# Kernel optimization log

Measured on AMD Instinct MI355X. Metric: run time of the kernel, lower is better.

Reference implementation:

```python
import jax, jax.numpy as jnp
import numpy as np
import math

C = 512          # channels
K = 3            # conv kernel size
DILATIONS = (1, 3, 5)
RATIO = 2        # up/down sample ratio
FK = 12          # FIR anti-alias kernel size


def kaiser_sinc_filter1d(cutoff, half_width, kernel_size):
    # BigVGAN alias-free kaiser-windowed sinc lowpass filter
    half_size = kernel_size // 2
    delta_f = 4.0 * half_width
    A = 2.285 * (half_size - 1) * math.pi * delta_f + 7.95
    if A > 50.0:
        beta = 0.1102 * (A - 8.7)
    elif A >= 21.0:
        beta = 0.5842 * (A - 21.0) ** 0.4 + 0.07886 * (A - 21.0)
    else:
        beta = 0.0
    window = np.kaiser(kernel_size, beta)
    if kernel_size % 2 == 0:
        time = np.arange(-half_size, half_size) + 0.5
    else:
        time = np.arange(kernel_size) - half_size
    filt = 2.0 * cutoff * window * np.sinc(2.0 * cutoff * time)
    filt = filt / filt.sum()
    return jnp.asarray(filt, dtype=jnp.float32)

# Up/Down both use cutoff=0.5/ratio, half_width=0.6/ratio, kernel=12
AA_FILTER = kaiser_sinc_filter1d(0.5 / RATIO, 0.6 / RATIO, FK)

UP_PAD = FK // RATIO - 1                               # 5 (replicate pad before transpose conv)
UP_PAD_LEFT = UP_PAD * RATIO + (FK - RATIO) // 2       # 15
UP_PAD_RIGHT = UP_PAD * RATIO + (FK - RATIO + 1) // 2  # 15
DN_PAD_LEFT = FK // 2 - 1                              # 5 (even kernel)
DN_PAD_RIGHT = FK // 2                                 # 6


def _depthwise_conv(x, filt, stride=1, lhs_dilation=1, padding=(0, 0)):
    c = x.shape[1]
    w = jnp.broadcast_to(filt.reshape(1, 1, -1), (c, 1, filt.shape[0]))
    return jax.lax.conv_general_dilated(
        x, w, window_strides=(stride,), padding=[padding],
        lhs_dilation=(lhs_dilation,), dimension_numbers=('NCH', 'OIH', 'NCH'),
        feature_group_count=c)


def upsample2x(x):
    # replicate pad, depthwise transposed conv (lhs-dilated conv w/ flipped kernel), crop, scale
    x = jnp.pad(x, ((0, 0), (0, 0), (UP_PAD, UP_PAD)), mode='edge')
    y = RATIO * _depthwise_conv(x, AA_FILTER[::-1], lhs_dilation=RATIO,
                                padding=(FK - 1, FK - 1))
    return y[..., UP_PAD_LEFT:-UP_PAD_RIGHT]


def downsample2x(x):
    x = jnp.pad(x, ((0, 0), (0, 0), (DN_PAD_LEFT, DN_PAD_RIGHT)), mode='edge')
    return _depthwise_conv(x, AA_FILTER, stride=RATIO)


def snake_log(x, alpha, beta):
    # use_log_scale=True: alpha/beta are exponentiated; x + 1/(b+1e-5) * sin(a*x)^2
    a = jnp.exp(alpha)[None, :, None]
    b = jnp.exp(beta)[None, :, None]
    return x + (1.0 / (b + 1e-5)) * jnp.square(jnp.sin(x * a))


def aliasing_activation(x, alpha, beta):
    return downsample2x(snake_log(upsample2x(x), alpha, beta))


def weight_norm_conv1d(x, v, g, bias, dilation):
    # torch weight_norm dim=0: W[o] = g[o] * v[o] / ||v[o]||
    norm = jnp.sqrt(jnp.sum(v * v, axis=(1, 2), keepdims=True))
    w = g[:, None, None] * v / norm
    pad = (K * dilation - dilation) // 2
    y = jax.lax.conv_general_dilated(
        x, w, window_strides=(1,), padding=[(pad, pad)],
        rhs_dilation=(dilation,), dimension_numbers=('NCH', 'OIH', 'NCH'))
    return y + bias[None, :, None]


def setup_inputs() -> dict:
    key = jax.random.key(0)
    ks = jax.random.split(key, 12)
    B, T = 16, 4096
    return {
        'x': jax.random.normal(ks[0], (B, C, T), dtype=jnp.float32),
        'float_masks': jnp.ones((B, 1, T), dtype=jnp.float32),
        'in_snake_alpha': 0.1 * jax.random.normal(ks[1], (3, C), dtype=jnp.float32),
        'in_snake_beta': 0.1 * jax.random.normal(ks[2], (3, C), dtype=jnp.float32),
        'out_snake_alpha': 0.1 * jax.random.normal(ks[3], (3, C), dtype=jnp.float32),
        'out_snake_beta': 0.1 * jax.random.normal(ks[4], (3, C), dtype=jnp.float32),
        'in_conv_v': 0.05 * jax.random.normal(ks[5], (3, C, C, K), dtype=jnp.float32),
        'in_conv_g': 1.0 + 0.01 * jax.random.normal(ks[6], (3, C), dtype=jnp.float32),
        'in_conv_b': 0.01 * jax.random.normal(ks[7], (3, C), dtype=jnp.float32),
        'out_conv_v': 0.05 * jax.random.normal(ks[8], (3, C, C, K), dtype=jnp.float32),
        'out_conv_g': 1.0 + 0.01 * jax.random.normal(ks[9], (3, C), dtype=jnp.float32),
        'out_conv_b': 0.01 * jax.random.normal(ks[10], (3, C), dtype=jnp.float32),
    }


def reference(x, float_masks, in_snake_alpha, in_snake_beta, out_snake_alpha,
              out_snake_beta, in_conv_v, in_conv_g, in_conv_b, out_conv_v,
              out_conv_g, out_conv_b):
    for i, dilation in enumerate(DILATIONS):
        residuals = x
        x = aliasing_activation(x, in_snake_alpha[i], in_snake_beta[i]) * float_masks
        x = weight_norm_conv1d(x, in_conv_v[i], in_conv_g[i], in_conv_b[i], dilation)
        x = aliasing_activation(x, out_snake_alpha[i], out_snake_beta[i]) * float_masks
        x = weight_norm_conv1d(x, out_conv_v[i], out_conv_g[i], out_conv_b[i], 1)
        x = x + residuals
    return x * float_masks
```

## Files before the change

### kernel.cpp

```cpp
#include <hip/hip_runtime.h>
#include <cmath>

#define BN_ 16
#define CN_ 512
#define TN_ 4096
#define TPAD_ 4112
#define PADR_ 8

typedef float f32x4 __attribute__((ext_vector_type(4)));
typedef __bf16 bf16x8 __attribute__((ext_vector_type(8)));
typedef unsigned short u16x8 __attribute__((ext_vector_type(8)));

struct AAFilt { float g0[6]; float g1[6]; float fE[6]; float fO[6]; };

__device__ __forceinline__ unsigned short f2bf(float f) {
  unsigned u = __builtin_bit_cast(unsigned, f);
  u = (u + 0x7fffu + ((u >> 16) & 1u)) >> 16;
  return (unsigned short)u;
}
__device__ __forceinline__ float bf2f(unsigned short h) {
  return __builtin_bit_cast(float, (unsigned)h << 16);
}

__device__ __forceinline__ void gld16(const void* g, void* l) {
  __builtin_amdgcn_global_load_lds((const __attribute__((address_space(1))) void*)g,
                                   (__attribute__((address_space(3))) void*)l,
                                   16, 0, 0);
}

__global__ __launch_bounds__(256) void prep_w(
    const float* __restrict__ vin, const float* __restrict__ gin,
    const float* __restrict__ vout, const float* __restrict__ gout,
    unsigned short* __restrict__ wpack)
{
  const int o = blockIdx.x;
  const int l = blockIdx.y;
  const int i = l >> 1, oc = l & 1;
  const float* v = (oc ? vout : vin) + (size_t)i * CN_ * CN_ * 3 + (size_t)o * CN_ * 3;
  const float g = (oc ? gout : gin)[i * CN_ + o];
  const int tid = threadIdx.x;

  float a = 0.f;
  for (int j = tid; j < 1536; j += 256) { float x = v[j]; a += x * x; }
  #pragma unroll
  for (int off = 32; off > 0; off >>= 1) a += __shfl_down(a, off);
  __shared__ float red[4];
  if ((tid & 63) == 0) red[tid >> 6] = a;
  __syncthreads();
  const float tot = red[0] + red[1] + red[2] + red[3];
  const float scale = g / sqrtf(tot);
  unsigned short* wl = wpack + (size_t)l * 3 * CN_ * CN_;
  for (int j = tid; j < 1536; j += 256) {
    int c = j / 3, k = j - 3 * c;
    wl[((size_t)k * CN_ + o) * CN_ + c] = f2bf(v[j] * scale);
  }
}

__global__ __launch_bounds__(256) void transpose_in(
    const float* __restrict__ src, unsigned short* __restrict__ dst)
{
  __shared__ float tile[32][33];
  const int b = blockIdx.z, c0 = blockIdx.y * 32, t0 = blockIdx.x * 32;
  const int tx = threadIdx.x & 31, ty = threadIdx.x >> 5;
  const float* s = src + ((size_t)b * CN_ + c0) * TN_ + t0;
  #pragma unroll
  for (int j = 0; j < 32; j += 8) tile[ty + j][tx] = s[(size_t)(ty + j) * TN_ + tx];
  __syncthreads();
  unsigned short* d = dst + ((size_t)b * TN_ + t0) * CN_ + c0;
  #pragma unroll
  for (int j = 0; j < 32; j += 8) d[(size_t)(ty + j) * CN_ + tx] = f2bf(tile[tx][ty + j]);
}

__global__ __launch_bounds__(512) void act_kernel(
    const unsigned short* __restrict__ src, unsigned short* __restrict__ dst,
    const float* __restrict__ alpha, const float* __restrict__ beta,
    const float* __restrict__ mask, AAFilt F)
{
  const int c = threadIdx.x;
  const int b = blockIdx.y;
  const int seg = blockIdx.x;
  const int t0 = seg << 7;
  const float av = expf(alpha[c]);
  const float ib = 1.0f / (expf(beta[c]) + 1e-5f);
  const unsigned short* row = src + (size_t)b * TN_ * CN_ + c;
  unsigned short* drow = dst + (size_t)b * TPAD_ * CN_ + c;
  const float* mrow = mask + (size_t)b * TN_;

  if (seg == 0)  { for (int p = 0; p < PADR_; ++p) drow[(size_t)p * CN_] = 0; }
  if (seg == 31) { for (int p = 0; p < PADR_; ++p) drow[(size_t)(TPAD_ - PADR_ + p) * CN_] = 0; }

  auto ldx = [&](int t) -> float {
    t = t < 0 ? 0 : (t > TN_ - 1 ? TN_ - 1 : t);
    return bf2f(row[(size_t)t * CN_]);
  };

  float xw[6];
  #pragma unroll
  for (int j = 0; j < 6; ++j) xw[j] = ldx(t0 - 5 + j);
  float sE[6], sO[6];
  #pragma unroll
  for (int j = 0; j < 6; ++j) { sE[j] = 0.f; sO[j] = 0.f; }
  float s_last = 0.f;

  auto step = [&](int tau, bool emit) {
    float uO = 0.f, uE = 0.f;
    #pragma unroll
    for (int j = 0; j < 6; ++j) { uO += F.g1[j] * xw[j]; uE += F.g0[j] * xw[j]; }
    float so = __sinf(uO * av); float sOn = uO + ib * so * so;
    float se = __sinf(uE * av); float sEn = uE + ib * se * se;
    if (tau + 2 == TN_ - 1) s_last = sOn;
    if (tau + 2 >= TN_) sOn = s_last;
    if (tau + 3 >= TN_) sEn = s_last;
    #pragma unroll
    for (int j = 0; j < 5; ++j) { sE[j] = sE[j + 1]; sO[j] = sO[j + 1]; }
    sE[5] = sEn; sO[5] = sOn;
    if (emit) {
      float d = 0.f;
      #pragma unroll
      for (int j = 0; j < 6; ++j) d += F.fE[j] * sE[j] + F.fO[j] * sO[j];
      d *= mrow[tau];
      drow[(size_t)(PADR_ + tau) * CN_] = f2bf(d);
    }
    #pragma unroll
    for (int j = 0; j < 5; ++j) xw[j] = xw[j + 1];
    xw[5] = ldx(tau + 6);
  };

  for (int w = 0; w < 5; ++w) step(t0 - 5 + w, false);
  if (t0 == 0) {
    float s0 = sE[3];
    sE[1] = s0; sE[2] = s0;
    sO[1] = s0; sO[2] = s0; sO[3] = s0;
  }
  for (int t = t0; t < t0 + 128; ++t) step(t, true);
}

#define ASZ (272 * 32)
#define BSZ (3 * 256 * 32)

#define VMCNT(n) asm volatile("s_waitcnt vmcnt(" #n ")" ::: "memory")
#define BAR __builtin_amdgcn_s_barrier()
#define PRIO1 __builtin_amdgcn_s_setprio(1)
#define PRIO0 __builtin_amdgcn_s_setprio(0)

#define READ_A(k, mlo) do { \
    const int rb_ = rbase[k] + (mlo) * 16; \
    const int q_ = q4 ^ ((rb_ >> 1) & 3); \
    const unsigned short* ap_ = A + ((size_t)rb_ * 4 + q_) * 8; \
    af[0] = __builtin_bit_cast(bf16x8, *(const u16x8*)(ap_)); \
    af[1] = __builtin_bit_cast(bf16x8, *(const u16x8*)(ap_ + 512)); \
    af[2] = __builtin_bit_cast(bf16x8, *(const u16x8*)(ap_ + 1024)); \
    af[3] = __builtin_bit_cast(bf16x8, *(const u16x8*)(ap_ + 1536)); \
  } while (0)

#define READ_B(k) do { \
    const int ob_ = wn * 64 + l15; \
    const int q_ = q4 ^ ((ob_ >> 1) & 3); \
    const unsigned short* bp_ = Bc + (((size_t)(k) * 256 + ob_) * 4 + q_) * 8; \
    bfr[0] = __builtin_bit_cast(bf16x8, *(const u16x8*)(bp_)); \
    bfr[1] = __builtin_bit_cast(bf16x8, *(const u16x8*)(bp_ + 512)); \
    bfr[2] = __builtin_bit_cast(bf16x8, *(const u16x8*)(bp_ + 1024)); \
    bfr[3] = __builtin_bit_cast(bf16x8, *(const u16x8*)(bp_ + 1536)); \
  } while (0)

#define MFMA16(mlo) do { \
    _Pragma("unroll") \
    for (int mi_ = 0; mi_ < 4; ++mi_) { \
      _Pragma("unroll") \
      for (int ni_ = 0; ni_ < 4; ++ni_) \
        acc[(mlo) + mi_][ni_] = __builtin_amdgcn_mfma_f32_16x16x32_bf16( \
            af[mi_], bfr[ni_], acc[(mlo) + mi_][ni_], 0, 0, 0); \
    } \
  } while (0)

template <int MODE, int DIL>
__global__ __launch_bounds__(512, 2) void conv_kernel(
    const unsigned short* __restrict__ act,
    const unsigned short* __restrict__ wp,
    const float* __restrict__ bias,
    const unsigned short* __restrict__ res,
    const float* __restrict__ mask,
    void* __restrict__ outp)
{
  __shared__ __align__(16) unsigned short lA[2 * ASZ];
  __shared__ __align__(16) unsigned short lB[2 * BSZ];

  const int tid = threadIdx.x;
  const int bid = blockIdx.x;
  const int xcd = bid & 7, j = bid >> 3;
  const int ob = j & 1, tile = j >> 1;
  const int tt = tile * 8 + xcd;
  const int b = tt >> 4;
  const int t0 = (tt & 15) << 8;
  const int o0 = ob << 8;

  const int lane = tid & 63;
  const int wave = tid >> 6;
  const int wm = wave >> 2, wn = wave & 3;
  const int l15 = lane & 15, q4 = lane >> 4;

  const f32x4 zero = {0.f, 0.f, 0.f, 0.f};
  f32x4 acc[8][4];
  #pragma unroll
  for (int a = 0; a < 8; ++a)
    #pragma unroll
    for (int n = 0; n < 4; ++n) acc[a][n] = zero;

  const unsigned short* aBase = act + ((size_t)b * TPAD_ + t0) * CN_;

  int rbase[3];
  #pragma unroll
  for (int k = 0; k < 3; ++k) rbase[k] = wm * 128 + l15 + PADR_ + (k - 1) * DIL;

  auto stageA = [&](unsigned short* Ad, int c0) {
    { int p = tid;       int r = p >> 2, pq = p & 3, gq = pq ^ ((r >> 1) & 3);
      gld16(aBase + (size_t)r * CN_ + c0 + gq * 8, Ad + (size_t)p * 8); }
    { int p = tid + 512; int r = p >> 2, pq = p & 3, gq = pq ^ ((r >> 1) & 3);
      gld16(aBase + (size_t)r * CN_ + c0 + gq * 8, Ad + (size_t)p * 8); }
    if (tid < 64) {
      int p = tid + 1024;
      int r = p >> 2, pq = p & 3, gq = pq ^ ((r >> 1) & 3);
      gld16(aBase + (size_t)r * CN_ + c0 + gq * 8, Ad + (size_t)p * 8); }
  };
  auto stageB = [&](unsigned short* Bd, int c0, int k) {
    { int p = tid;       int ol = p >> 2, pq = p & 3, gq = pq ^ ((ol >> 1) & 3);
      gld16(wp + ((size_t)(k * CN_) + o0 + ol) * CN_ + c0 + gq * 8,
            Bd + ((size_t)k * 1024 + p) * 8); }
    { int p = tid + 512; int ol = p >> 2, pq = p & 3, gq = pq ^ ((ol >> 1) & 3);
      gld16(wp + ((size_t)(k * CN_) + o0 + ol) * CN_ + c0 + gq * 8,
            Bd + ((size_t)k * 1024 + p) * 8); }
  };

  stageA(lA, 0); stageB(lB, 0, 0); stageB(lB, 0, 1); stageB(lB, 0, 2);
  VMCNT(4);
  BAR;

  for (int cb = 0; cb < 15; ++cb) {
    const unsigned short* A  = lA + (size_t)(cb & 1) * ASZ;
    const unsigned short* Bc = lB + (size_t)(cb & 1) * BSZ;
    unsigned short* An = lA + (size_t)((cb & 1) ^ 1) * ASZ;
    unsigned short* Bn = lB + (size_t)((cb & 1) ^ 1) * BSZ;
    const int c0n = (cb + 1) * 32;
    bf16x8 af[4], bfr[4];
    READ_A(0, 0); READ_B(0); stageA(An, c0n);
    BAR; PRIO1; MFMA16(0); PRIO0; BAR;
    READ_A(0, 4); stageB(Bn, c0n, 0);
    BAR; PRIO1; MFMA16(4); PRIO0; VMCNT(6); BAR;
    READ_A(1, 0); READ_B(1); stageB(Bn, c0n, 1);
    BAR; PRIO1; MFMA16(0); PRIO0; BAR;
    READ_A(1, 4); stageB(Bn, c0n, 2);
    BAR; PRIO1; MFMA16(4); PRIO0; VMCNT(6); BAR;
    READ_A(2, 0); READ_B(2);
    BAR; PRIO1; MFMA16(0); PRIO0; BAR;
    READ_A(2, 4);
    BAR; PRIO1; MFMA16(4); PRIO0; VMCNT(4); BAR;
  }
  {
    const unsigned short* A  = lA + ASZ;
    const unsigned short* Bc = lB + BSZ;
    bf16x8 af[4], bfr[4];
    READ_A(0, 0); READ_B(0);
    BAR; PRIO1; MFMA16(0); PRIO0; BAR;
    READ_A(0, 4);
    BAR; PRIO1; MFMA16(4); PRIO0; VMCNT(2); BAR;
    READ_A(1, 0); READ_B(1);
    BAR; PRIO1; MFMA16(0); PRIO0; BAR;
    READ_A(1, 4);
    BAR; PRIO1; MFMA16(4); PRIO0; VMCNT(0); BAR;
    READ_A(2, 0); READ_B(2);
    BAR; PRIO1; MFMA16(0); PRIO0; BAR;
    READ_A(2, 4);
    BAR; PRIO1; MFMA16(4); PRIO0;
  }

  const int obase = o0 + wn * 64 + l15;
  const int tbase = t0 + wm * 128 + q4 * 4;

  if (MODE == 0) {
    unsigned short* O = (unsigned short*)outp + (size_t)b * TN_ * CN_;
    #pragma unroll
    for (int ni = 0; ni < 4; ++ni) {
      float bv = bias[obase + ni * 16];
      #pragma unroll
      for (int mi = 0; mi < 8; ++mi) {
        #pragma unroll
        for (int r = 0; r < 4; ++r) {
          int t = tbase + mi * 16 + r;
          O[(size_t)t * CN_ + obase + ni * 16] = f2bf(acc[mi][ni][r] + bv);
        }
      }
    }
  } else if (MODE == 1) {
    unsigned short* O = (unsigned short*)outp + (size_t)b * TN_ * CN_;
    const unsigned short* R = res + (size_t)b * TN_ * CN_;
    #pragma unroll
    for (int ni = 0; ni < 4; ++ni) {
      float bv = bias[obase + ni * 16];
      #pragma unroll
      for (int mi = 0; mi < 8; ++mi) {
        #pragma unroll
        for (int r = 0; r < 4; ++r) {
          int t = tbase + mi * 16 + r;
          size_t ix = (size_t)t * CN_ + obase + ni * 16;
          O[ix] = f2bf(acc[mi][ni][r] + bv + bf2f(R[ix]));
        }
      }
    }
  } else {
    float* O = (float*)outp + (size_t)b * CN_ * TN_;
    const unsigned short* R = res + (size_t)b * TN_ * CN_;
    const float* M = mask + (size_t)b * TN_;
    float bv[4];
    #pragma unroll
    for (int ni = 0; ni < 4; ++ni) bv[ni] = bias[obase + ni * 16];
    #pragma unroll
    for (int mi = 0; mi < 8; ++mi) {
      int t = tbase + mi * 16;
      f32x4 mv = *reinterpret_cast<const f32x4*>(M + t);
      #pragma unroll
      for (int ni = 0; ni < 4; ++ni) {
        f32x4 v;
        #pragma unroll
        for (int r = 0; r < 4; ++r)
          v[r] = (acc[mi][ni][r] + bv[ni] + bf2f(R[(size_t)(t + r) * CN_ + obase + ni * 16])) * mv[r];
        *reinterpret_cast<f32x4*>(O + (size_t)(obase + ni * 16) * TN_ + t) = v;
      }
    }
  }
}

static double bi0(double x) {
  double s = 1.0, t = 1.0, q = x * x * 0.25;
  for (int k = 1; k < 50; ++k) { t *= q / ((double)k * (double)k); s += t; if (t < 1e-18 * s) break; }
  return s;
}
static void make_filt(AAFilt* F) {
  const double PI = 3.14159265358979323846;
  double A = 2.285 * 5.0 * PI * 1.2 + 7.95;
  double beta;
  if (A > 50.0) beta = 0.1102 * (A - 8.7);
  else if (A >= 21.0) beta = 0.5842 * pow(A - 21.0, 0.4) + 0.07886 * (A - 21.0);
  else beta = 0.0;
  double i0b = bi0(beta);
  double f[12], sum = 0.0;
  for (int n = 0; n < 12; ++n) {
    double xx = 2.0 * n / 11.0 - 1.0;
    double w = bi0(beta * sqrt(fmax(0.0, 1.0 - xx * xx))) / i0b;
    double tt = (double)(n - 6) + 0.5;
    double arg = 0.5 * tt;
    double snc = sin(PI * arg) / (PI * arg);
    f[n] = 0.5 * w * snc;
    sum += f[n];
  }
  for (int n = 0; n < 12; ++n) f[n] /= sum;
  for (int j = 0; j < 6; ++j) {
    F->g0[j] = (float)(2.0 * f[11 - 2 * j]);
    F->g1[j] = (float)(2.0 * f[10 - 2 * j]);
    F->fE[j] = (float)f[2 * j + 1];
    F->fO[j] = (float)f[2 * j];
  }
}

extern "C" void kernel_launch(void* const* d_in, const int* in_sizes, int n_in,
                              void* d_out, int out_size, void* d_ws, size_t ws_size,
                              hipStream_t stream)
{
  (void)in_sizes; (void)n_in; (void)out_size; (void)ws_size;
  const float* x    = (const float*)d_in[0];
  const float* mask = (const float*)d_in[1];
  const float* inA  = (const float*)d_in[2];
  const float* inB  = (const float*)d_in[3];
  const float* outA = (const float*)d_in[4];
  const float* outB = (const float*)d_in[5];
  const float* vin  = (const float*)d_in[6];
  const float* gin  = (const float*)d_in[7];
  const float* bin  = (const float*)d_in[8];
  const float* vout = (const float*)d_in[9];
  const float* gout = (const float*)d_in[10];
  const float* bout = (const float*)d_in[11];

  char* ws = (char*)d_ws;
  unsigned short* xta  = (unsigned short*)ws;
  unsigned short* xtb  = (unsigned short*)(ws + 67108864);
  unsigned short* actb = (unsigned short*)(ws + 134217728);
  unsigned short* y1   = (unsigned short*)(ws + 134217728 + 67371008);
  unsigned short* wpk  = (unsigned short*)(ws + 134217728 + 67371008 + 67108864);

  AAFilt F; make_filt(&F);

  prep_w<<<dim3(512, 6), dim3(256), 0, stream>>>(vin, gin, vout, gout, wpk);
  transpose_in<<<dim3(128, 16, 16), dim3(256), 0, stream>>>(x, xta);

  act_kernel<<<dim3(32, 16), dim3(512), 0, stream>>>(
      xta, actb, inA + 0 * CN_, inB + 0 * CN_, mask, F);
  conv_kernel<0, 1><<<dim3(512), dim3(512), 0, stream>>>(
      actb, wpk + (size_t)0 * 3 * CN_ * CN_, bin + 0 * CN_, nullptr, mask, (void*)y1);
  act_kernel<<<dim3(32, 16), dim3(512), 0, stream>>>(
      y1, actb, outA + 0 * CN_, outB + 0 * CN_, mask, F);
  conv_kernel<1, 1><<<dim3(512), dim3(512), 0, stream>>>(
      actb, wpk + (size_t)1 * 3 * CN_ * CN_, bout + 0 * CN_, xta, mask, (void*)xtb);

  act_kernel<<<dim3(32, 16), dim3(512), 0, stream>>>(
      xtb, actb, inA + 1 * CN_, inB + 1 * CN_, mask, F);
  conv_kernel<0, 3><<<dim3(512), dim3(512), 0, stream>>>(
      actb, wpk + (size_t)2 * 3 * CN_ * CN_, bin + 1 * CN_, nullptr, mask, (void*)y1);
  act_kernel<<<dim3(32, 16), dim3(512), 0, stream>>>(
      y1, actb, outA + 1 * CN_, outB + 1 * CN_, mask, F);
  conv_kernel<1, 1><<<dim3(512), dim3(512), 0, stream>>>(
      actb, wpk + (size_t)3 * 3 * CN_ * CN_, bout + 1 * CN_, xtb, mask, (void*)xta);

  act_kernel<<<dim3(32, 16), dim3(512), 0, stream>>>(
      xta, actb, inA + 2 * CN_, inB + 2 * CN_, mask, F);
  conv_kernel<0, 5><<<dim3(512), dim3(512), 0, stream>>>(
      actb, wpk + (size_t)4 * 3 * CN_ * CN_, bin + 2 * CN_, nullptr, mask, (void*)y1);
  act_kernel<<<dim3(32, 16), dim3(512), 0, stream>>>(
      y1, actb, outA + 2 * CN_, outB + 2 * CN_, mask, F);
  conv_kernel<2, 1><<<dim3(512), dim3(512), 0, stream>>>(
      actb, wpk + (size_t)5 * 3 * CN_ * CN_, bout + 2 * CN_, xta, mask, d_out);
}
```

Before: 1.150 ms.

## Restructure conv GEMM main loop into 64-channel k-tiles with per-tap A staging

```diff
diff --git a/kernel.cpp b/kernel.cpp
--- a/kernel.cpp
+++ b/kernel.cpp
@@ -1,5 +1,6 @@
 #include <hip/hip_runtime.h>
 #include <cmath>
+#include <cstddef>
 
 #define BN_ 16
 #define CN_ 512
@@ -135,41 +136,50 @@
   for (int t = t0; t < t0 + 128; ++t) step(t, true);
 }
 
-#define ASZ (272 * 32)
-#define BSZ (3 * 256 * 32)
+#define HSZ 8192
+#define TSZ 16384
 
 #define VMCNT(n) asm volatile("s_waitcnt vmcnt(" #n ")" ::: "memory")
 #define BAR __builtin_amdgcn_s_barrier()
 #define PRIO1 __builtin_amdgcn_s_setprio(1)
 #define PRIO0 __builtin_amdgcn_s_setprio(0)
 
-#define READ_A(k, mlo) do { \
-    const int rb_ = rbase[k] + (mlo) * 16; \
-    const int q_ = q4 ^ ((rb_ >> 1) & 3); \
-    const unsigned short* ap_ = A + ((size_t)rb_ * 4 + q_) * 8; \
-    af[0] = __builtin_bit_cast(bf16x8, *(const u16x8*)(ap_)); \
-    af[1] = __builtin_bit_cast(bf16x8, *(const u16x8*)(ap_ + 512)); \
-    af[2] = __builtin_bit_cast(bf16x8, *(const u16x8*)(ap_ + 1024)); \
-    af[3] = __builtin_bit_cast(bf16x8, *(const u16x8*)(ap_ + 1536)); \
+#define READ_A(base, mh) do { \
+    _Pragma("unroll") \
+    for (int mi_ = 0; mi_ < 4; ++mi_) { \
+      const int row_ = wm * 128 + (mh) * 64 + mi_ * 16 + l15; \
+      _Pragma("unroll") \
+      for (int kk_ = 0; kk_ < 2; ++kk_) { \
+        const int q_ = (q4 + kk_ * 4) ^ (row_ & 7); \
+        af[mi_][kk_] = __builtin_bit_cast(bf16x8, \
+            *(const u16x8*)((base) + (size_t)row_ * 64 + q_ * 8)); \
+      } \
+    } \
   } while (0)
 
-#define READ_B(k) do { \
-    const int ob_ = wn * 64 + l15; \
-    const int q_ = q4 ^ ((ob_ >> 1) & 3); \
-    const unsigned short* bp_ = Bc + (((size_t)(k) * 256 + ob_) * 4 + q_) * 8; \
-    bfr[0] = __builtin_bit_cast(bf16x8, *(const u16x8*)(bp_)); \
-    bfr[1] = __builtin_bit_cast(bf16x8, *(const u16x8*)(bp_ + 512)); \
-    bfr[2] = __builtin_bit_cast(bf16x8, *(const u16x8*)(bp_ + 1024)); \
-    bfr[3] = __builtin_bit_cast(bf16x8, *(const u16x8*)(bp_ + 1536)); \
+#define READ_B(base, nh) do { \
+    _Pragma("unroll") \
+    for (int ni_ = 0; ni_ < 2; ++ni_) { \
+      const int orow_ = wn * 64 + ((nh) * 2 + ni_) * 16 + l15; \
+      _Pragma("unroll") \
+      for (int kk_ = 0; kk_ < 2; ++kk_) { \
+        const int q_ = (q4 + kk_ * 4) ^ (orow_ & 7); \
+        bfr[ni_][kk_] = __builtin_bit_cast(bf16x8, \
+            *(const u16x8*)((base) + (size_t)orow_ * 64 + q_ * 8)); \
+      } \
+    } \
   } while (0)
 
-#define MFMA16(mlo) do { \
+#define MFMA16(mh, nh) do { \
     _Pragma("unroll") \
     for (int mi_ = 0; mi_ < 4; ++mi_) { \
       _Pragma("unroll") \
-      for (int ni_ = 0; ni_ < 4; ++ni_) \
-        acc[(mlo) + mi_][ni_] = __builtin_amdgcn_mfma_f32_16x16x32_bf16( \
-            af[mi_], bfr[ni_], acc[(mlo) + mi_][ni_], 0, 0, 0); \
+      for (int ni_ = 0; ni_ < 2; ++ni_) { \
+        acc[(mh) * 4 + mi_][(nh) * 2 + ni_] = __builtin_amdgcn_mfma_f32_16x16x32_bf16( \
+            af[mi_][0], bfr[ni_][0], acc[(mh) * 4 + mi_][(nh) * 2 + ni_], 0, 0, 0); \
+        acc[(mh) * 4 + mi_][(nh) * 2 + ni_] = __builtin_amdgcn_mfma_f32_16x16x32_bf16( \
+            af[mi_][1], bfr[ni_][1], acc[(mh) * 4 + mi_][(nh) * 2 + ni_], 0, 0, 0); \
+      } \
     } \
   } while (0)
 
@@ -182,8 +192,8 @@
     const float* __restrict__ mask,
     void* __restrict__ outp)
 {
-  __shared__ __align__(16) unsigned short lA[2 * ASZ];
-  __shared__ __align__(16) unsigned short lB[2 * BSZ];
+  __shared__ __align__(16) unsigned short lA[2 * TSZ];
+  __shared__ __align__(16) unsigned short lB[2 * TSZ];
 
   const int tid = threadIdx.x;
   const int bid = blockIdx.x;
@@ -206,72 +216,65 @@
     #pragma unroll
     for (int n = 0; n < 4; ++n) acc[a][n] = zero;
 
-  const unsigned short* aBase = act + ((size_t)b * TPAD_ + t0) * CN_;
-
-  int rbase[3];
-  #pragma unroll
-  for (int k = 0; k < 3; ++k) rbase[k] = wm * 128 + l15 + PADR_ + (k - 1) * DIL;
-
-  auto stageA = [&](unsigned short* Ad, int c0) {
-    { int p = tid;       int r = p >> 2, pq = p & 3, gq = pq ^ ((r >> 1) & 3);
-      gld16(aBase + (size_t)r * CN_ + c0 + gq * 8, Ad + (size_t)p * 8); }
-    { int p = tid + 512; int r = p >> 2, pq = p & 3, gq = pq ^ ((r >> 1) & 3);
-      gld16(aBase + (size_t)r * CN_ + c0 + gq * 8, Ad + (size_t)p * 8); }
-    if (tid < 64) {
-      int p = tid + 1024;
-      int r = p >> 2, pq = p & 3, gq = pq ^ ((r >> 1) & 3);
-      gld16(aBase + (size_t)r * CN_ + c0 + gq * 8, Ad + (size_t)p * 8); }
+  const unsigned short* aBaseP = act + ((size_t)b * TPAD_ + t0 + PADR_) * CN_;
+
+  unsigned short* const Ab[2] = { lA, lA + TSZ };
+  unsigned short* const Bb[2] = { lB, lB + TSZ };
+
+  auto stageA = [&](unsigned short* bufBase, int kappa, int half) {
+    const int cb = kappa / 3, k = kappa - 3 * cb;
+    const unsigned short* src = aBaseP
+        + (ptrdiff_t)((k - 1) * DIL + half * 128) * CN_ + cb * 64;
+    unsigned short* dst = bufBase + (size_t)half * HSZ;
+    #pragma unroll
+    for (int s = 0; s < 2; ++s) {
+      int p = tid + (s << 9);
+      int rih = p >> 3, pq = p & 7;
+      int gq = pq ^ (rih & 7);
+      gld16(src + (size_t)rih * CN_ + gq * 8, dst + (size_t)p * 8);
+    }
   };
-  auto stageB = [&](unsigned short* Bd, int c0, int k) {
-    { int p = tid;       int ol = p >> 2, pq = p & 3, gq = pq ^ ((ol >> 1) & 3);
-      gld16(wp + ((size_t)(k * CN_) + o0 + ol) * CN_ + c0 + gq * 8,
-            Bd + ((size_t)k * 1024 + p) * 8); }
-    { int p = tid + 512; int ol = p >> 2, pq = p & 3, gq = pq ^ ((ol >> 1) & 3);
-      gld16(wp + ((size_t)(k * CN_) + o0 + ol) * CN_ + c0 + gq * 8,
-            Bd + ((size_t)k * 1024 + p) * 8); }
+  auto stageB = [&](unsigned short* bufBase, int kappa, int half) {
+    const int cb = kappa / 3, k = kappa - 3 * cb;
+    const unsigned short* src = wp
+        + ((size_t)k * CN_ + o0 + half * 128) * CN_ + cb * 64;
+    unsigned short* dst = bufBase + (size_t)half * HSZ;
+    #pragma unroll
+    for (int s = 0; s < 2; ++s) {
+      int p = tid + (s << 9);
+      int rih = p >> 3, pq = p & 7;
+      int gq = pq ^ (rih & 7);
+      gld16(src + (size_t)rih * CN_ + gq * 8, dst + (size_t)p * 8);
+    }
   };
 
-  stageA(lA, 0); stageB(lB, 0, 0); stageB(lB, 0, 1); stageB(lB, 0, 2);
-  VMCNT(4);
+  stageA(Ab[0], 0, 0); stageA(Ab[0], 0, 1);
+  stageB(Bb[0], 0, 0); stageB(Bb[0], 0, 1);
+  stageB(Bb[1], 1, 1);
+  VMCNT(2);
   BAR;
 
-  for (int cb = 0; cb < 15; ++cb) {
-    const unsigned short* A  = lA + (size_t)(cb & 1) * ASZ;
-    const unsigned short* Bc = lB + (size_t)(cb & 1) * BSZ;
-    unsigned short* An = lA + (size_t)((cb & 1) ^ 1) * ASZ;
-    unsigned short* Bn = lB + (size_t)((cb & 1) ^ 1) * BSZ;
-    const int c0n = (cb + 1) * 32;
-    bf16x8 af[4], bfr[4];
-    READ_A(0, 0); READ_B(0); stageA(An, c0n);
-    BAR; PRIO1; MFMA16(0); PRIO0; BAR;
-    READ_A(0, 4); stageB(Bn, c0n, 0);
-    BAR; PRIO1; MFMA16(4); PRIO0; VMCNT(6); BAR;
-    READ_A(1, 0); READ_B(1); stageB(Bn, c0n, 1);
-    BAR; PRIO1; MFMA16(0); PRIO0; BAR;
-    READ_A(1, 4); stageB(Bn, c0n, 2);
-    BAR; PRIO1; MFMA16(4); PRIO0; VMCNT(6); BAR;
-    READ_A(2, 0); READ_B(2);
-    BAR; PRIO1; MFMA16(0); PRIO0; BAR;
-    READ_A(2, 4);
-    BAR; PRIO1; MFMA16(4); PRIO0; VMCNT(4); BAR;
-  }
-  {
-    const unsigned short* A  = lA + ASZ;
-    const unsigned short* Bc = lB + BSZ;
-    bf16x8 af[4], bfr[4];
-    READ_A(0, 0); READ_B(0);
-    BAR; PRIO1; MFMA16(0); PRIO0; BAR;
-    READ_A(0, 4);
-    BAR; PRIO1; MFMA16(4); PRIO0; VMCNT(2); BAR;
-    READ_A(1, 0); READ_B(1);
-    BAR; PRIO1; MFMA16(0); PRIO0; BAR;
-    READ_A(1, 4);
-    BAR; PRIO1; MFMA16(4); PRIO0; VMCNT(0); BAR;
-    READ_A(2, 0); READ_B(2);
-    BAR; PRIO1; MFMA16(0); PRIO0; BAR;
-    READ_A(2, 4);
-    BAR; PRIO1; MFMA16(4); PRIO0;
-  }
+  for (int i = 0; i < 12; ++i) {
+    const int kt1 = 2 * i + 1, ktn = 2 * i + 2, ktn1 = 2 * i + 3;
+    bf16x8 af[4][2], bfr[2][2];
+    READ_A(Ab[0], 0); READ_B(Bb[0], 0); stageA(Ab[1], kt1, 0);
+    BAR; PRIO1; MFMA16(0, 0); PRIO0; BAR;
+    READ_A(Ab[0], 1); stageA(Ab[1], kt1, 1);
+    BAR; PRIO1; MFMA16(1, 0); PRIO0; BAR;
+    READ_A(Ab[0], 0); READ_B(Bb[0], 1); stageB(Bb[1], kt1, 0);
+    BAR; PRIO1; MFMA16(0, 1); PRIO0; BAR;
+    READ_A(Ab[0], 1); stageB(Bb[0], ktn, 0);
+    BAR; PRIO1; MFMA16(1, 1); PRIO0; VMCNT(2); BAR;
+    READ_A(Ab[1], 0); READ_B(Bb[1], 0); stageA(Ab[0], ktn, 0);
+    BAR; PRIO1; MFMA16(0, 0); PRIO0; BAR;
+    READ_A(Ab[1], 1); stageA(Ab[0], ktn, 1);
+    BAR; PRIO1; MFMA16(1, 0); PRIO0; BAR;
+    READ_A(Ab[1], 0); READ_B(Bb[1], 1); stageB(Bb[0], ktn, 1);
+    BAR; PRIO1; MFMA16(0, 1); PRIO0; BAR;
+    READ_A(Ab[1], 1); stageB(Bb[1], ktn1, 1);
+    BAR; PRIO1; MFMA16(1, 1); PRIO0; VMCNT(2); BAR;
+  }
+  VMCNT(0);
 
   const int obase = o0 + wn * 64 + l15;
   const int tbase = t0 + wm * 128 + q4 * 4;
```

New measurement: 1.303 ms. 13.3% more time.
